# Kernel optimization log

Hardware: AMD Instinct MI355X
Metric: run time of the kernel (lower is better)

## Reference

```python
import jax, jax.numpy as jnp
import numpy as np

# 3-21G hydrogen basis: shell 1 = 2 primitives, shell 2 = 1 primitive (padded with coeff 0)
# basis-function order: atom0 shell0, atom0 shell1, atom1 shell0, atom1 shell1
_EXPS = jnp.array([[5.4471780, 0.8245472],
                   [0.1831916, 1.0],
                   [5.4471780, 0.8245472],
                   [0.1831916, 1.0]], dtype=jnp.float32)
_COEF = jnp.array([[0.1562850, 0.9046910],
                   [1.0, 0.0],
                   [0.1562850, 0.9046910],
                   [1.0, 0.0]], dtype=jnp.float32)
_ZS = jnp.array([1.0, 1.0], dtype=jnp.float32)  # nuclear charges
_NOCC = 1        # 2 electrons -> 1 doubly-occupied MO
_N_SCF = 30      # fixed SCF iterations (jit-friendly)


def _f0(t):
    # Boys function F0(t) = 0.5*sqrt(pi/t)*erf(sqrt(t)), with small-t expansion
    ts = jnp.maximum(t, 1e-12)
    big = 0.5 * jnp.sqrt(jnp.pi / ts) * jax.scipy.special.erf(jnp.sqrt(ts))
    return jnp.where(t < 1e-10, 1.0 - t / 3.0, big)


def setup_inputs() -> dict:
    # H2 geometry from the source module (bohr)
    atom_position = jnp.array([[1.0, 0.0, 0.0], [-1.0, 0.0, 0.0]], dtype=jnp.float32)
    return {"atom_position": atom_position}


def reference(atom_position):
    R = atom_position                                   # (2,3) nuclear coords
    centers = R[jnp.array([0, 0, 1, 1])]                # (4,3) per-bf centers
    a = _EXPS                                           # (4,2)
    c = _COEF * (2.0 * _EXPS / jnp.pi) ** 0.75          # primitive-normalized coeffs

    ai = a[:, :, None, None]                            # (4,2,1,1)
    aj = a[None, None, :, :]                            # (1,1,4,2)
    Ri = centers[:, None, None, None, :]                # (4,1,1,1,3)
    Rj = centers[None, None, :, None, :]                # (1,1,4,1,3)
    p = ai + aj                                         # (4,2,4,2)
    mu = ai * aj / p
    Rij2 = jnp.sum((Ri - Rj) ** 2, -1)                  # (4,1,4,1)
    K = jnp.exp(-mu * Rij2)                             # (4,2,4,2)
    Sprim = (jnp.pi / p) ** 1.5 * K

    # renormalize contracted functions to unit self-overlap
    Sc = jnp.einsum('ip,jq,ipjq->ij', c, c, Sprim)
    c = c * (1.0 / jnp.sqrt(jnp.diag(Sc)))[:, None]

    S = jnp.einsum('ip,jq,ipjq->ij', c, c, Sprim)       # overlap (4,4)
    Tprim = mu * (3.0 - 2.0 * mu * Rij2) * Sprim
    T = jnp.einsum('ip,jq,ipjq->ij', c, c, Tprim)       # kinetic (4,4)

    # Gaussian product center P (4,2,4,2,3)
    P = (ai[..., None] * Ri + aj[..., None] * Rj) / p[..., None]
    PC2 = jnp.sum((P[..., None, :] - R) ** 2, -1)       # (4,2,4,2,2)
    Vprim = -(2.0 * jnp.pi / p[..., None]) * K[..., None] * _ZS \
            * _f0(p[..., None] * PC2)
    V = jnp.einsum('ip,jq,ipjq->ij', c, c, jnp.sum(Vprim, -1))

    # two-electron integrals (ij|kl), all s-type -> single Boys F0
    pb = p[:, :, :, :, None, None, None, None]
    qk = p[None, None, None, None, :, :, :, :]
    PQ2 = jnp.sum((P[:, :, :, :, None, None, None, None, :]
                   - P[None, None, None, None, :, :, :, :, :]) ** 2, -1)
    alpha = pb * qk / (pb + qk)
    Gprim = (2.0 * jnp.pi ** 2.5) / (pb * qk * jnp.sqrt(pb + qk)) \
            * K[:, :, :, :, None, None, None, None] \
            * K[None, None, None, None, :, :, :, :] \
            * _f0(alpha * PQ2)
    ERI = jnp.einsum('ip,jq,kr,ls,ipjqkrls->ijkl', c, c, c, c, Gprim)  # (4,4,4,4)

    Hc = T + V
    s_val, s_vec = jnp.linalg.eigh(S)
    X = (s_vec * (s_val ** -0.5)) @ s_vec.T             # symmetric orthogonalizer

    def fock(D):
        J = jnp.einsum('kl,ijkl->ij', D, ERI)
        Kx = jnp.einsum('kl,ikjl->ij', D, ERI)
        return Hc + J - 0.5 * Kx

    def scf_step(D, _):
        F = fock(D)
        Fp = X.T @ F @ X
        _, Cp = jnp.linalg.eigh(Fp)
        C = X @ Cp
        Cocc = C[:, :_NOCC]
        return 2.0 * Cocc @ Cocc.T, None

    D0 = jnp.zeros((4, 4), dtype=Hc.dtype)
    D, _ = jax.lax.scan(scf_step, D0, None, length=_N_SCF)

    F = fock(D)
    e_elec = 0.5 * jnp.sum(D * (Hc + F))
    e_nuc = _ZS[0] * _ZS[1] / jnp.linalg.norm(R[0] - R[1])
    return e_elec + e_nuc
```

## Files before the change

kernel.cpp:

```cpp
#include <hip/hip_runtime.h>
#include <math.h>

#define PI_F 3.14159265358979323846f

__device__ __constant__ float c_EX[8] = {5.447178f, 0.8245472f, 0.1831916f, 1.0f,
                                         5.447178f, 0.8245472f, 0.1831916f, 1.0f};
__device__ __constant__ float c_NC[8] = {0.39715137f, 0.55792070f, 0.19956670f, 0.0f,
                                         0.39715137f, 0.55792070f, 0.19956670f, 0.0f};

__device__ __forceinline__ float frcp(float x) { return __builtin_amdgcn_rcpf(x); }
__device__ __forceinline__ float frsq(float x) { return __builtin_amdgcn_rsqf(x); }

__device__ __forceinline__ float f0f(float tv) {
    float ts = fmaxf(tv, 1e-12f);
    float st = sqrtf(ts);
    float u = frcp(fmaf(0.3275911f, st, 1.0f));
    float c = fmaf(u, 1.061405429f, -1.453152027f);
    c = fmaf(u, c, 1.421413741f);
    c = fmaf(u, c, -0.284496736f);
    c = fmaf(u, c, 0.254829592f);
    float poly = c * u;
    float ex = __expf(-ts);
    float big = 0.88622692545f * frcp(st) * (1.0f - poly * ex);
    float ser = fmaf(tv, fmaf(tv, 0.1f, -0.3333333333f), 1.0f);
    return (tv < 0.01f) ? ser : big;
}

__device__ __forceinline__ void pairAB(int p, int& a, int& b) {
    a = (p < 4) ? 0 : ((p < 7) ? 1 : ((p < 9) ? 2 : 3));
    b = p - ((p < 4) ? 0 : ((p < 7) ? 3 : ((p < 9) ? 5 : 6)));
}

__global__ __launch_bounds__(128, 1) void hf_h2_kernel(const float* __restrict__ R,
                                                       float* __restrict__ out) {
    __shared__ float pp[64], pW[64], pPx[64], pPy[64], pPz[64];
    __shared__ float pSp[64], pTp[64], pVp[64];
    __shared__ float sSm[16], sTm[16], sVm[16], sN[4], sHc[16];
    __shared__ float sE2[110], sERI[256], sTa[128], sTb[48];
    __shared__ float sU[4], sT6[6], sHp[3];

    const int t = threadIdx.x;

    if (t < 64) {
        int u = t >> 3, v = t & 7;
        float au = c_EX[u], av = c_EX[v];
        float cc = c_NC[u] * c_NC[v];
        int atu = (u >> 2) * 3, atv = (v >> 2) * 3;
        float ux = R[atu + 0], uy = R[atu + 1], uz = R[atu + 2];
        float vx = R[atv + 0], vy = R[atv + 1], vz = R[atv + 2];
        float ps = au + av;
        float inv = frcp(ps);
        float mu = au * av * inv;
        float dx = ux - vx, dy = uy - vy, dz = uz - vz;
        float r2 = dx * dx + dy * dy + dz * dz;
        float Kab = __expf(-mu * r2);
        float Px = (au * ux + av * vx) * inv;
        float Py = (au * uy + av * vy) * inv;
        float Pz = (au * uz + av * vz) * inv;
        float pio = PI_F * inv;
        float Sp = pio * sqrtf(pio) * Kab;
        float Tp = mu * (3.0f - 2.0f * mu * r2) * Sp;
        float d0x = Px - R[0], d0y = Py - R[1], d0z = Pz - R[2];
        float d1x = Px - R[3], d1y = Py - R[4], d1z = Pz - R[5];
        float pc0 = d0x * d0x + d0y * d0y + d0z * d0z;
        float pc1 = d1x * d1x + d1y * d1y + d1z * d1z;
        float Vp = -(2.0f * PI_F * inv) * Kab * (f0f(ps * pc0) + f0f(ps * pc1));
        pp[t] = ps; pW[t] = cc * Kab;
        pPx[t] = Px; pPy[t] = Py; pPz[t] = Pz;
        pSp[t] = cc * Sp; pTp[t] = cc * Tp; pVp[t] = cc * Vp;
    }
    __syncthreads();

    int ui = 0, uj = 0, uk = 0, ul = 0;
    if (t < 110) {
        int tt = (t < 55) ? t : t - 55;
        int P = (tt >= 10) + (tt >= 19) + (tt >= 27) + (tt >= 34) + (tt >= 40)
              + (tt >= 45) + (tt >= 49) + (tt >= 52) + (tt >= 54);
        int base = P * 10 - ((P * (P - 1)) >> 1);
        int Q = tt - base + P;
        pairAB(P, ui, uj);
        pairAB(Q, uk, ul);
        int nbase = (t >= 55) ? 2 : 0;
        float sum = 0.0f;
        #pragma unroll
        for (int nn = 0; nn < 2; ++nn) {
            int n = nbase + nn;
            int p = n >> 1, q = n & 1;
            int b1 = (ui * 2 + p) * 8 + uj * 2 + q;
            float p1 = pp[b1], W1 = pW[b1];
            float x1 = pPx[b1], y1 = pPy[b1], z1 = pPz[b1];
            #pragma unroll 2
            for (int m = 0; m < 4; ++m) {
                int r = m >> 1, s2 = m & 1;
                int b2 = (uk * 2 + r) * 8 + ul * 2 + s2;
                float p2 = pp[b2];
                float psum = p1 + p2;
                float dx = x1 - pPx[b2], dy = y1 - pPy[b2], dz = z1 - pPz[b2];
                float pq2 = dx * dx + dy * dy + dz * dz;
                float p12 = p1 * p2;
                float invs = frsq(psum);
                float al = p12 * invs * invs;
                float gf = 34.98683665f * frcp(p12) * invs;
                sum += W1 * pW[b2] * gf * f0f(al * pq2);
            }
        }
        sE2[t] = sum;
    } else if (t < 126) {
        int m = t - 110;
        int i = m >> 2, j = m & 3;
        float aS = 0.0f, aT = 0.0f, aV = 0.0f;
        #pragma unroll
        for (int p = 0; p < 2; ++p)
        #pragma unroll
        for (int q = 0; q < 2; ++q) {
            int b = (i * 2 + p) * 8 + (j * 2 + q);
            aS += pSp[b]; aT += pTp[b]; aV += pVp[b];
        }
        sSm[m] = aS; sTm[m] = aT; sVm[m] = aV;
        if (i == j) sN[i] = frsq(aS);
    }
    __syncthreads();

    if (t < 55) {
        float v = (sE2[t] + sE2[t + 55]) * sN[ui] * sN[uj] * sN[uk] * sN[ul];
        int i = ui, j = uj, k = uk, l = ul;
        sERI[((i * 4 + j) * 4 + k) * 4 + l] = v;
        sERI[((j * 4 + i) * 4 + k) * 4 + l] = v;
        sERI[((i * 4 + j) * 4 + l) * 4 + k] = v;
        sERI[((j * 4 + i) * 4 + l) * 4 + k] = v;
        sERI[((k * 4 + l) * 4 + i) * 4 + j] = v;
        sERI[((l * 4 + k) * 4 + i) * 4 + j] = v;
        sERI[((k * 4 + l) * 4 + j) * 4 + i] = v;
        sERI[((l * 4 + k) * 4 + j) * 4 + i] = v;
    } else if (t >= 64 && t < 80) {
        int m = t - 64;
        int i = m >> 2, j = m & 3;
        sHc[m] = (sTm[m] + sVm[m]) * sN[i] * sN[j];
    } else if (t >= 96 && t < 100) {
        float n0 = sN[0], n1 = sN[1], n2 = sN[2], n3 = sN[3];
        float a = sSm[1] * n0 * n1;
        float b = sSm[2] * n0 * n2;
        float cb = 0.5f * (sSm[3] * n0 * n3 + sSm[6] * n1 * n2);
        float d = sSm[7] * n1 * n3;
        float p2 = 2.0f * (1.0f + b), q2 = 2.0f * (1.0f + d), r2 = 2.0f * (a + cb);
        float h = 0.5f * (p2 - q2);
        float mm = 0.5f * (p2 + q2);
        float rt = fmaxf(sqrtf(fmaf(h, h, r2 * r2)), 1e-20f);
        float i1 = frsq(mm + rt), i2 = frsq(mm - rt);
        float irt = frcp(rt);
        float c2f = 0.5f * fmaf(h, irt, 1.0f);
        float s2f = 0.5f * fmaf(-h, irt, 1.0f);
        float csf = 0.5f * r2 * irt;
        int idx = t - 96;
        float val = (idx == 0) ? (c2f * i1 + s2f * i2)
                  : (idx == 3) ? (s2f * i1 + c2f * i2)
                               : (csf * (i1 - i2));
        sU[idx] = val;
    }
    __syncthreads();

    {
        int m = t >> 6, low = t & 63;
        float s = 0.0f;
        #pragma unroll
        for (int i = 0; i < 4; ++i)
            s = fmaf(sU[(i & 1) * 2 + m], sERI[i * 64 + low], s);
        sTa[t] = s;
    }
    __syncthreads();

    if (t < 48) {
        int p = t >> 4, kl = t & 15;
        int m = p >> 1, n = (p + 1) >> 1;
        float s = 0.0f;
        #pragma unroll
        for (int j = 0; j < 4; ++j)
            s = fmaf(sU[(j & 1) * 2 + n], sTa[m * 64 + j * 16 + kl], s);
        sTb[t] = s;
    }
    __syncthreads();

    if (t < 6) {
        int P = (t < 3) ? 0 : ((t < 5) ? 1 : 2);
        int Q = t - ((t < 3) ? 0 : ((t < 5) ? 2 : 3));
        int a = Q >> 1, b = (Q + 1) >> 1;
        float s = 0.0f;
        #pragma unroll
        for (int k = 0; k < 4; ++k) {
            float inner = 0.0f;
            #pragma unroll
            for (int l = 0; l < 4; ++l)
                inner = fmaf(sU[(l & 1) * 2 + b], sTb[P * 16 + k * 4 + l], inner);
            s = fmaf(sU[(k & 1) * 2 + a], inner, s);
        }
        sT6[t] = s;
    } else if (t >= 8 && t < 11) {
        int p = t - 8;
        int a = p >> 1, b = (p + 1) >> 1;
        float s = 0.0f;
        #pragma unroll
        for (int i = 0; i < 4; ++i) {
            float inner = 0.0f;
            #pragma unroll
            for (int j = 0; j < 4; ++j)
                inner = fmaf(sU[(j & 1) * 2 + b], sHc[i * 4 + j], inner);
            s = fmaf(sU[(i & 1) * 2 + a], inner, s);
        }
        sHp[p] = s;
    }
    __syncthreads();

    {
        float T0 = sT6[0], T1v = sT6[1], T2v = sT6[2];
        float T3v = sT6[3], T4v = sT6[4], T5v = sT6[5];
        float H0 = sHp[0], H1 = sHp[1], H2 = sHp[2];
        float G00 = T0,              G01 = 2.0f * T1v,      G02 = 2.0f * T2v - T3v;
        float G10 = T1v,             G11 = 3.0f * T3v - T2v, G12 = T4v;
        float G20 = G02,             G21 = 2.0f * T4v,      G22 = T5v;

        float f0 = H0, f1 = H1, f2 = H2;
        float w0 = 0.0f, w1 = 0.0f, w2 = 0.0f;
        #pragma unroll 1
        for (int it = 0; it < 10; ++it) {
            float h = 0.5f * (f0 - f2);
            float rt = sqrtf(fmaf(h, h, f1 * f1));
            float va = (h >= 0.0f) ? f1 : (h - rt);
            float vb = (h >= 0.0f) ? (-(h + rt)) : f1;
            float rn = frsq(fmaf(va, va, vb * vb));
            float v1 = va * rn, v2 = vb * rn;
            w0 = v1 * v1; w1 = v1 * v2; w2 = v2 * v2;
            f0 = fmaf(G00, w0, fmaf(G01, w1, fmaf(G02, w2, H0)));
            f1 = fmaf(G10, w0, fmaf(G11, w1, fmaf(G12, w2, H1)));
            f2 = fmaf(G20, w0, fmaf(G21, w1, fmaf(G22, w2, H2)));
        }
        float e = (H0 + f0) * w0 + 2.0f * (H1 + f1) * w1 + (H2 + f2) * w2;
        float dx = R[0] - R[3], dy = R[1] - R[4], dz = R[2] - R[5];
        e += frsq(dx * dx + dy * dy + dz * dz);
        if (t == 0) out[0] = e;
    }
}

extern "C" void kernel_launch(void* const* d_in, const int* in_sizes, int n_in,
                              void* d_out, int out_size, void* d_ws, size_t ws_size,
                              hipStream_t stream) {
    const float* R = (const float*)d_in[0];
    float* out = (float*)d_out;
    hf_h2_kernel<<<1, 128, 0, stream>>>(R, out);
}
```

Baseline: 9.848 us.

## Split ERI primitive loop across four waves and collapse basis transform stages

Launches 256 threads so each of four waves computes one outer primitive pair of the two-electron integrals, which shortens the serial loop per thread. The one-electron contractions move onto the spare lanes. The three-stage ERI transform by the symmetric orthogonalizer is replaced by a 16-entry pre-reduction that folds the atom-symmetric structure of the transform matrix, followed by a direct contraction. This removes two barrier-separated stages. In exchange it doubles the block size and relies on the orthogonalizer's specific block structure.

```diff
diff --git a/kernel.cpp b/kernel.cpp
--- a/kernel.cpp
+++ b/kernel.cpp
@@ -31,15 +31,17 @@
     b = p - ((p < 4) ? 0 : ((p < 7) ? 3 : ((p < 9) ? 5 : 6)));
 }
 
-__global__ __launch_bounds__(128, 1) void hf_h2_kernel(const float* __restrict__ R,
+__global__ __launch_bounds__(256, 1) void hf_h2_kernel(const float* __restrict__ R,
                                                        float* __restrict__ out) {
     __shared__ float pp[64], pW[64], pPx[64], pPy[64], pPz[64];
     __shared__ float pSp[64], pTp[64], pVp[64];
     __shared__ float sSm[16], sTm[16], sVm[16], sN[4], sHc[16];
-    __shared__ float sE2[110], sERI[256], sTa[128], sTb[48];
-    __shared__ float sU[4], sT6[6], sHp[3];
+    __shared__ float sE4[220], sERI[256];
+    __shared__ float sU[4], sEr[16], sHr[4], sT6[6], sHp[3];
 
     const int t = threadIdx.x;
+    const int w = t >> 6;
+    const int tt = t & 63;
 
     if (t < 64) {
         int u = t >> 3, v = t & 7;
@@ -72,57 +74,54 @@
     __syncthreads();
 
     int ui = 0, uj = 0, uk = 0, ul = 0;
-    if (t < 110) {
-        int tt = (t < 55) ? t : t - 55;
+    if (tt < 55) {
         int P = (tt >= 10) + (tt >= 19) + (tt >= 27) + (tt >= 34) + (tt >= 40)
               + (tt >= 45) + (tt >= 49) + (tt >= 52) + (tt >= 54);
         int base = P * 10 - ((P * (P - 1)) >> 1);
         int Q = tt - base + P;
         pairAB(P, ui, uj);
         pairAB(Q, uk, ul);
-        int nbase = (t >= 55) ? 2 : 0;
+        int p = w >> 1, q = w & 1;
+        int b1 = (ui * 2 + p) * 8 + uj * 2 + q;
+        float p1 = pp[b1], W1 = pW[b1];
+        float x1 = pPx[b1], y1 = pPy[b1], z1 = pPz[b1];
         float sum = 0.0f;
-        #pragma unroll
-        for (int nn = 0; nn < 2; ++nn) {
-            int n = nbase + nn;
-            int p = n >> 1, q = n & 1;
-            int b1 = (ui * 2 + p) * 8 + uj * 2 + q;
-            float p1 = pp[b1], W1 = pW[b1];
-            float x1 = pPx[b1], y1 = pPy[b1], z1 = pPz[b1];
-            #pragma unroll 2
-            for (int m = 0; m < 4; ++m) {
-                int r = m >> 1, s2 = m & 1;
-                int b2 = (uk * 2 + r) * 8 + ul * 2 + s2;
-                float p2 = pp[b2];
-                float psum = p1 + p2;
-                float dx = x1 - pPx[b2], dy = y1 - pPy[b2], dz = z1 - pPz[b2];
-                float pq2 = dx * dx + dy * dy + dz * dz;
-                float p12 = p1 * p2;
-                float invs = frsq(psum);
-                float al = p12 * invs * invs;
-                float gf = 34.98683665f * frcp(p12) * invs;
-                sum += W1 * pW[b2] * gf * f0f(al * pq2);
+        #pragma unroll 2
+        for (int m = 0; m < 4; ++m) {
+            int r = m >> 1, s2 = m & 1;
+            int b2 = (uk * 2 + r) * 8 + ul * 2 + s2;
+            float p2 = pp[b2];
+            float psum = p1 + p2;
+            float dx = x1 - pPx[b2], dy = y1 - pPy[b2], dz = z1 - pPz[b2];
+            float pq2 = dx * dx + dy * dy + dz * dz;
+            float p12 = p1 * p2;
+            float invs = frsq(psum);
+            float al = p12 * invs * invs;
+            float gf = 34.98683665f * frcp(p12) * invs;
+            sum += W1 * pW[b2] * gf * f0f(al * pq2);
+        }
+        sE4[w * 55 + tt] = sum;
+    } else {
+        int m = w * 9 + (tt - 55);
+        if (m < 16) {
+            int i = m >> 2, j = m & 3;
+            float aS = 0.0f, aT = 0.0f, aV = 0.0f;
+            #pragma unroll
+            for (int p = 0; p < 2; ++p)
+            #pragma unroll
+            for (int q = 0; q < 2; ++q) {
+                int b = (i * 2 + p) * 8 + (j * 2 + q);
+                aS += pSp[b]; aT += pTp[b]; aV += pVp[b];
             }
-        }
-        sE2[t] = sum;
-    } else if (t < 126) {
-        int m = t - 110;
-        int i = m >> 2, j = m & 3;
-        float aS = 0.0f, aT = 0.0f, aV = 0.0f;
-        #pragma unroll
-        for (int p = 0; p < 2; ++p)
-        #pragma unroll
-        for (int q = 0; q < 2; ++q) {
-            int b = (i * 2 + p) * 8 + (j * 2 + q);
-            aS += pSp[b]; aT += pTp[b]; aV += pVp[b];
-        }
-        sSm[m] = aS; sTm[m] = aT; sVm[m] = aV;
-        if (i == j) sN[i] = frsq(aS);
+            sSm[m] = aS; sTm[m] = aT; sVm[m] = aV;
+            if (i == j) sN[i] = frsq(aS);
+        }
     }
     __syncthreads();
 
     if (t < 55) {
-        float v = (sE2[t] + sE2[t + 55]) * sN[ui] * sN[uj] * sN[uk] * sN[ul];
+        float v = (sE4[t] + sE4[55 + t] + sE4[110 + t] + sE4[165 + t])
+                * sN[ui] * sN[uj] * sN[uk] * sN[ul];
         int i = ui, j = uj, k = uk, l = ul;
         sERI[((i * 4 + j) * 4 + k) * 4 + l] = v;
         sERI[((j * 4 + i) * 4 + k) * 4 + l] = v;
@@ -159,39 +158,44 @@
     }
     __syncthreads();
 
-    {
-        int m = t >> 6, low = t & 63;
+    if (t < 16) {
+        int al = (t >> 3) & 1, be = (t >> 2) & 1, ga = (t >> 1) & 1, de = t & 1;
         float s = 0.0f;
         #pragma unroll
-        for (int i = 0; i < 4; ++i)
-            s = fmaf(sU[(i & 1) * 2 + m], sERI[i * 64 + low], s);
-        sTa[t] = s;
-    }
-    __syncthreads();
-
-    if (t < 48) {
-        int p = t >> 4, kl = t & 15;
-        int m = p >> 1, n = (p + 1) >> 1;
-        float s = 0.0f;
-        #pragma unroll
-        for (int j = 0; j < 4; ++j)
-            s = fmaf(sU[(j & 1) * 2 + n], sTa[m * 64 + j * 16 + kl], s);
-        sTb[t] = s;
+        for (int i2 = 0; i2 < 2; ++i2)
+        #pragma unroll
+        for (int j2 = 0; j2 < 2; ++j2)
+        #pragma unroll
+        for (int k2 = 0; k2 < 2; ++k2)
+        #pragma unroll
+        for (int l2 = 0; l2 < 2; ++l2)
+            s += sERI[((al + 2 * i2) * 4 + (be + 2 * j2)) * 16
+                      + (ga + 2 * k2) * 4 + (de + 2 * l2)];
+        sEr[t] = s;
+    } else if (t < 20) {
+        int c = t - 16;
+        int al = (c >> 1) & 1, be = c & 1;
+        sHr[c] = sHc[al * 4 + be] + sHc[al * 4 + be + 2]
+               + sHc[(al + 2) * 4 + be] + sHc[(al + 2) * 4 + be + 2];
     }
     __syncthreads();
 
     if (t < 6) {
         int P = (t < 3) ? 0 : ((t < 5) ? 1 : 2);
         int Q = t - ((t < 3) ? 0 : ((t < 5) ? 2 : 3));
-        int a = Q >> 1, b = (Q + 1) >> 1;
+        int a = P >> 1, b = (P + 1) >> 1, c = Q >> 1, d = (Q + 1) >> 1;
         float s = 0.0f;
         #pragma unroll
-        for (int k = 0; k < 4; ++k) {
-            float inner = 0.0f;
-            #pragma unroll
-            for (int l = 0; l < 4; ++l)
-                inner = fmaf(sU[(l & 1) * 2 + b], sTb[P * 16 + k * 4 + l], inner);
-            s = fmaf(sU[(k & 1) * 2 + a], inner, s);
+        for (int al = 0; al < 2; ++al)
+        #pragma unroll
+        for (int be = 0; be < 2; ++be) {
+            float L = sU[al * 2 + a] * sU[be * 2 + b];
+            #pragma unroll
+            for (int ga = 0; ga < 2; ++ga)
+            #pragma unroll
+            for (int de = 0; de < 2; ++de)
+                s = fmaf(L * (sU[ga * 2 + c] * sU[de * 2 + d]),
+                         sEr[al * 8 + be * 4 + ga * 2 + de], s);
         }
         sT6[t] = s;
     } else if (t >= 8 && t < 11) {
@@ -199,13 +203,10 @@
         int a = p >> 1, b = (p + 1) >> 1;
         float s = 0.0f;
         #pragma unroll
-        for (int i = 0; i < 4; ++i) {
-            float inner = 0.0f;
-            #pragma unroll
-            for (int j = 0; j < 4; ++j)
-                inner = fmaf(sU[(j & 1) * 2 + b], sHc[i * 4 + j], inner);
-            s = fmaf(sU[(i & 1) * 2 + a], inner, s);
-        }
+        for (int al = 0; al < 2; ++al)
+        #pragma unroll
+        for (int be = 0; be < 2; ++be)
+            s = fmaf(sU[al * 2 + a] * sU[be * 2 + b], sHr[al * 2 + be], s);
         sHp[p] = s;
     }
     __syncthreads();
@@ -214,9 +215,9 @@
         float T0 = sT6[0], T1v = sT6[1], T2v = sT6[2];
         float T3v = sT6[3], T4v = sT6[4], T5v = sT6[5];
         float H0 = sHp[0], H1 = sHp[1], H2 = sHp[2];
-        float G00 = T0,              G01 = 2.0f * T1v,      G02 = 2.0f * T2v - T3v;
-        float G10 = T1v,             G11 = 3.0f * T3v - T2v, G12 = T4v;
-        float G20 = G02,             G21 = 2.0f * T4v,      G22 = T5v;
+        float G00 = T0,   G01 = 2.0f * T1v,       G02 = 2.0f * T2v - T3v;
+        float G10 = T1v,  G11 = 3.0f * T3v - T2v, G12 = T4v;
+        float G20 = G02,  G21 = 2.0f * T4v,       G22 = T5v;
 
         float f0 = H0, f1 = H1, f2 = H2;
         float w0 = 0.0f, w1 = 0.0f, w2 = 0.0f;
@@ -245,5 +246,5 @@
                               hipStream_t stream) {
     const float* R = (const float*)d_in[0];
     float* out = (float*)d_out;
-    hf_h2_kernel<<<1, 128, 0, stream>>>(R, out);
-}
+    hf_h2_kernel<<<1, 256, 0, stream>>>(R, out);
+}
```

Measured after the change: 9.290 us. 1.06x faster.
